# Optimization experiments

Hardware: AMD Instinct MI355X
Metric: run time of the kernel (lower is better)

## Reference

```python
import math
import jax, jax.numpy as jnp
import numpy as np

BLOCK_K = 128  # key/value block size; S_k % BLOCK_K == 0 so no padding/mask needed


def setup_inputs() -> dict:
    key = jax.random.key(0)
    kq, kk, kv = jax.random.split(key, 3)
    B, S, H, Hkv, D = 1, 4096, 16, 8, 128
    return {
        "query": jax.random.normal(kq, (B, S, H, D), dtype=jnp.float32),
        "key": jax.random.normal(kk, (B, S, Hkv, D), dtype=jnp.float32),
        "value": jax.random.normal(kv, (B, S, Hkv, D), dtype=jnp.float32),
    }


def _ring_attention(query, key, value, block_k=BLOCK_K):
    # query: [B, Sq, H, D]; key/value: [B, Sk, Hkv, D]
    scale = 1.0 / math.sqrt(query.shape[-1])
    reps = query.shape[2] // key.shape[2]
    if reps > 1:  # GQA: repeat kv heads to match query heads
        key = jnp.repeat(key, reps, axis=2)
        value = jnp.repeat(value, reps, axis=2)
    q = jnp.transpose(query, (0, 2, 1, 3))   # [B, H, Sq, D]
    k = jnp.transpose(key, (0, 2, 1, 3))     # [B, H, Sk, D]
    v = jnp.transpose(value, (0, 2, 1, 3))
    B, H, Sq, D = q.shape
    Sk = k.shape[2]
    nk = Sk // block_k
    # split keys/values into blocks, block axis leading for scan
    kb = k.reshape(B, H, nk, block_k, D).transpose(2, 0, 1, 3, 4)
    vb = v.reshape(B, H, nk, block_k, D).transpose(2, 0, 1, 3, 4)
    m0 = jnp.full((B, H, Sq), -jnp.inf, dtype=jnp.float32)
    l0 = jnp.zeros((B, H, Sq), dtype=jnp.float32)
    o0 = jnp.zeros((B, H, Sq, D), dtype=jnp.float32)

    def step(carry, kv_blk):
        m, l, o = carry
        k_blk, v_blk = kv_blk
        scores = jnp.einsum('bhqd,bhkd->bhqk', q, k_blk) * scale
        m_new = jnp.maximum(m, jnp.max(scores, axis=-1))
        alpha = jnp.exp(m - m_new)                     # rescale factor (0 on first step)
        p = jnp.exp(scores - m_new[..., None])
        l = l * alpha + jnp.sum(p, axis=-1)
        o = o * alpha[..., None] + jnp.einsum('bhqk,bhkd->bhqd', p, v_blk)
        return (m_new, l, o), None

    (m, l, o), _ = jax.lax.scan(step, (m0, l0, o0), (kb, vb))
    out = o / l[..., None]
    return jnp.transpose(out, (0, 2, 1, 3))  # [B, Sq, H, D]


def reference(query, key, value):
    return _ring_attention(query, key, value)
```

## Files before the change

kernel.cpp:

```cpp
#include <hip/hip_runtime.h>
#include <math.h>


namespace {
constexpr int NH  = 16;
constexpr int NKV = 8;
constexpr int DH  = 128;
constexpr int SK  = 4096;
constexpr int TQ  = 128;
constexpr int NT  = 256;

constexpr int BKM   = 32;
constexpr int NKTM  = SK / BKM;
constexpr int TILEM = BKM * DH;
constexpr size_t WS_NEED = (size_t)2 * NKV * NKTM * TILEM * sizeof(_Float16);

constexpr int BK  = 64;
constexpr int NKT = SK / BK;

typedef _Float16 half8 __attribute__((ext_vector_type(8)));
typedef _Float16 half4 __attribute__((ext_vector_type(4)));
typedef _Float16 half2v __attribute__((ext_vector_type(2)));
typedef __fp16   fp16x2 __attribute__((ext_vector_type(2)));
typedef float  floatx4 __attribute__((ext_vector_type(4)));
typedef unsigned short ushort8 __attribute__((ext_vector_type(8)));

#define MFMA16(a, b, c) __builtin_amdgcn_mfma_f32_16x16x32_f16((a), (b), (c), 0, 0, 0)

__global__ __launch_bounds__(256)
void prepack_kv(const float* __restrict__ Kg, const float* __restrict__ Vg,
                _Float16* __restrict__ Kx, _Float16* __restrict__ Vx) {
  __shared__ __align__(16) _Float16 Kb[BKM * 128];
  __shared__ __align__(16) _Float16 Vb[BKM * 132];
  const int id = blockIdx.x;
  const int hk = id & 7;
  const int kt = id >> 3;
  const int t  = threadIdx.x;

#pragma unroll
  for (int it = 0; it < 4; ++it) {
    const int r  = it * 8 + (t >> 5);
    const int c4 = t & 31;
    const size_t src = (((size_t)(kt * BKM + r) * NKV + hk) * DH) + c4 * 4;
    const float4 kf = *reinterpret_cast<const float4*>(Kg + src);
    const float4 vf = *reinterpret_cast<const float4*>(Vg + src);
    half4 kh;
    kh[0] = (_Float16)kf.x; kh[1] = (_Float16)kf.y;
    kh[2] = (_Float16)kf.z; kh[3] = (_Float16)kf.w;
    *reinterpret_cast<half4*>(&Kb[r * 128 + c4 * 4]) = kh;
    half2v v0, v1;
    v0[0] = (_Float16)vf.x; v0[1] = (_Float16)vf.y;
    v1[0] = (_Float16)vf.z; v1[1] = (_Float16)vf.w;
    *reinterpret_cast<half2v*>(&Vb[r * 132 + c4 * 4])     = v0;
    *reinterpret_cast<half2v*>(&Vb[r * 132 + c4 * 4 + 2]) = v1;
  }
  __syncthreads();

  {
    _Float16* out = Kx + (size_t)(hk * NKTM + kt) * TILEM;
#pragma unroll
    for (int it = 0; it < 2; ++it) {
      const int L  = it * 2048 + t * 8;
      const int r  = L >> 7;
      const int gp = (L >> 3) & 15;
      const int c8 = gp ^ (r & 7);
      *reinterpret_cast<half8*>(out + L) =
          *reinterpret_cast<const half8*>(&Kb[r * 128 + c8 * 8]);
    }
  }
  {
    _Float16* out = Vx + (size_t)(hk * NKTM + kt) * TILEM;
    const int dp = t >> 2;
    const int g  = t & 3;
    const int ql = g ^ (dp & 3);
    const int d  = dp * 2;
    ushort8 lo, hi;
#pragma unroll
    for (int j = 0; j < 8; ++j) {
      const int key = ((j >> 2) * 16) + ql * 4 + (j & 3);
      const unsigned v = *reinterpret_cast<const unsigned*>(&Vb[key * 132 + d]);
      lo[j] = (unsigned short)(v & 0xffffu);
      hi[j] = (unsigned short)(v >> 16);
    }
    *reinterpret_cast<ushort8*>(out + d * 32 + g * 8)       = lo;
    *reinterpret_cast<ushort8*>(out + (d + 1) * 32 + g * 8) = hi;
  }
}

__global__ __launch_bounds__(NT, 2)
void flash_fwd_pk(const float* __restrict__ Qg,
                  const _Float16* __restrict__ Kx,
                  const _Float16* __restrict__ Vx,
                  float* __restrict__ Og) {
  __shared__ __align__(16) _Float16 KsB[2][TILEM];
  __shared__ __align__(16) _Float16 VtB[2][TILEM];

  const int tid  = threadIdx.x;
  const int wave = tid >> 6;
  const int lane = tid & 63;
  const int m16  = lane & 15;
  const int quad = lane >> 4;
  const int hsw  = m16 & 7;
  const int sw2  = (m16 >> 1) & 3;

  const int id = blockIdx.x;
  const int hk = id & 7;
  const int h  = (hk << 1) | ((id >> 3) & 1);
  const int qt = id >> 4;
  const int qr0 = qt * TQ + wave * 32;

  const float4* Q4 = reinterpret_cast<const float4*>(Qg);
  const float scale2 = (float)(0.08838834764831845 * 1.4426950408889634);

  half8 qa[2][4];
#pragma unroll
  for (int mt = 0; mt < 2; ++mt) {
#pragma unroll
    for (int kc = 0; kc < 4; ++kc) {
      const int r = qr0 + mt * 16 + m16;
      const int b = (r * NH + h) * (DH / 4) + kc * 8 + quad * 2;
      float4 x = Q4[b], y = Q4[b + 1];
      half8 f;
      f[0] = (_Float16)(x.x * scale2); f[1] = (_Float16)(x.y * scale2);
      f[2] = (_Float16)(x.z * scale2); f[3] = (_Float16)(x.w * scale2);
      f[4] = (_Float16)(y.x * scale2); f[5] = (_Float16)(y.y * scale2);
      f[6] = (_Float16)(y.z * scale2); f[7] = (_Float16)(y.w * scale2);
      qa[mt][kc] = f;
    }
  }

  floatx4 o[2][8];
#pragma unroll
  for (int mt = 0; mt < 2; ++mt)
#pragma unroll
    for (int nt = 0; nt < 8; ++nt) o[mt][nt] = (floatx4){0.f, 0.f, 0.f, 0.f};
  float lsum[2] = {0.f, 0.f};

  const _Float16* gK = Kx + (size_t)hk * NKTM * TILEM;
  const _Float16* gV = Vx + (size_t)hk * NKTM * TILEM;
  const int soff = tid * 8;

  half8 kr[2], vr[2];
#pragma unroll
  for (int i = 0; i < 2; ++i) {
    kr[i] = *reinterpret_cast<const half8*>(gK + i * 2048 + soff);
    vr[i] = *reinterpret_cast<const half8*>(gV + i * 2048 + soff);
  }

  for (int kt = 0; kt < NKTM; ++kt) {
    const int b = kt & 1;
#pragma unroll
    for (int i = 0; i < 2; ++i) {
      *reinterpret_cast<half8*>(&KsB[b][i * 2048 + soff]) = kr[i];
      *reinterpret_cast<half8*>(&VtB[b][i * 2048 + soff]) = vr[i];
    }
    {
      const int ktn = (kt + 1 < NKTM) ? kt + 1 : kt;
      const _Float16* gKt = gK + (size_t)ktn * TILEM;
      const _Float16* gVt = gV + (size_t)ktn * TILEM;
#pragma unroll
      for (int i = 0; i < 2; ++i) {
        kr[i] = *reinterpret_cast<const half8*>(gKt + i * 2048 + soff);
        vr[i] = *reinterpret_cast<const half8*>(gVt + i * 2048 + soff);
      }
    }
    __syncthreads();

    const _Float16* Ks = KsB[b];
    const _Float16* Vt = VtB[b];

    floatx4 s[2][2];
#pragma unroll
    for (int mt = 0; mt < 2; ++mt)
#pragma unroll
      for (int nt = 0; nt < 2; ++nt) s[mt][nt] = (floatx4){0.f, 0.f, 0.f, 0.f};
#pragma unroll
    for (int nt = 0; nt < 2; ++nt) {
#pragma unroll
      for (int kc = 0; kc < 4; ++kc) {
        const int g = (kc * 4 + quad) ^ hsw;
        half8 kb = *reinterpret_cast<const half8*>(
            &Ks[(nt * 16 + m16) * 128 + g * 8]);
        s[0][nt] = MFMA16(kb, qa[0][nt * 0 + kc], s[0][nt]);
        s[1][nt] = MFMA16(kb, qa[1][kc], s[1][nt]);
      }
    }

    union H8 { half8 h; fp16x2 w[4]; };
    half8 pa[2];
#pragma unroll
    for (int mt = 0; mt < 2; ++mt) {
      float p[8];
#pragma unroll
      for (int nt = 0; nt < 2; ++nt)
#pragma unroll
        for (int r = 0; r < 4; ++r)
          p[nt * 4 + r] = __builtin_amdgcn_exp2f(s[mt][nt][r]);
      lsum[mt] += ((p[0] + p[1]) + (p[2] + p[3])) +
                  ((p[4] + p[5]) + (p[6] + p[7]));
      H8 u;
      u.w[0] = __builtin_amdgcn_cvt_pkrtz(p[0], p[1]);
      u.w[1] = __builtin_amdgcn_cvt_pkrtz(p[2], p[3]);
      u.w[2] = __builtin_amdgcn_cvt_pkrtz(p[4], p[5]);
      u.w[3] = __builtin_amdgcn_cvt_pkrtz(p[6], p[7]);
      pa[mt] = u.h;
    }

    const int gq = quad ^ sw2;
#pragma unroll
    for (int nt = 0; nt < 8; ++nt) {
      half8 vb = *reinterpret_cast<const half8*>(
          &Vt[(nt * 16 + m16) * 32 + gq * 8]);
      o[0][nt] = MFMA16(pa[0], vb, o[0][nt]);
      o[1][nt] = MFMA16(pa[1], vb, o[1][nt]);
    }
  }

#pragma unroll
  for (int mt = 0; mt < 2; ++mt) {
    float ls = lsum[mt];
    ls += __shfl_xor(ls, 16);
    ls += __shfl_xor(ls, 32);
#pragma unroll
    for (int r = 0; r < 4; ++r) {
      const int rq = quad * 4 + r;
      const float inv = 1.f / __shfl(ls, rq);
      const int row = qr0 + mt * 16 + rq;
      const int ob = (row * NH + h) * DH + m16;
#pragma unroll
      for (int nt = 0; nt < 8; ++nt)
        Og[ob + nt * 16] = o[mt][nt][r] * inv;
    }
  }
}

constexpr int KP = 136, VP = 72, PP = 72;

__global__ __launch_bounds__(NT, 2)
void flash_fwd_fb(const float* __restrict__ Qg, const float* __restrict__ Kg,
                  const float* __restrict__ Vg, float* __restrict__ Og) {
  __shared__ _Float16 Ks[BK * KP];
  __shared__ _Float16 Vt[DH * VP];
  __shared__ _Float16 Ps[4 * 32 * PP];

  const int tid  = threadIdx.x;
  const int wave = tid >> 6;
  const int lane = tid & 63;
  const int m16  = lane & 15;
  const int quad = lane >> 4;

  const int id = blockIdx.x;
  const int hk = id & 7;
  const int h  = (hk << 1) | ((id >> 3) & 1);
  const int qt = id >> 4;
  const int qr0 = qt * TQ + wave * 32;

  const float4* Q4 = reinterpret_cast<const float4*>(Qg);
  const float4* K4 = reinterpret_cast<const float4*>(Kg);
  const float scale2 = (float)(0.08838834764831845 * 1.4426950408889634);

  half8 qa[2][4];
#pragma unroll
  for (int mt = 0; mt < 2; ++mt) {
#pragma unroll
    for (int kc = 0; kc < 4; ++kc) {
      const int r = qr0 + mt * 16 + m16;
      const int b = (r * NH + h) * (DH / 4) + kc * 8 + quad * 2;
      float4 x = Q4[b], y = Q4[b + 1];
      half8 f;
      f[0] = (_Float16)(x.x * scale2); f[1] = (_Float16)(x.y * scale2);
      f[2] = (_Float16)(x.z * scale2); f[3] = (_Float16)(x.w * scale2);
      f[4] = (_Float16)(y.x * scale2); f[5] = (_Float16)(y.y * scale2);
      f[6] = (_Float16)(y.z * scale2); f[7] = (_Float16)(y.w * scale2);
      qa[mt][kc] = f;
    }
  }

  floatx4 o[2][8];
#pragma unroll
  for (int mt = 0; mt < 2; ++mt)
#pragma unroll
    for (int nt = 0; nt < 8; ++nt) o[mt][nt] = (floatx4){0.f, 0.f, 0.f, 0.f};
  float lrow[2][4];
#pragma unroll
  for (int mt = 0; mt < 2; ++mt)
#pragma unroll
    for (int r = 0; r < 4; ++r) lrow[mt][r] = 0.f;

  const int kkey = tid >> 2, kdq = tid & 3;
  const int vdim = tid & 127, vkg = tid >> 7;

  float4 kpre[8];
  float  vpre[32];
  {
    const int kb = (kkey * NKV + hk) * (DH / 4);
#pragma unroll
    for (int j = 0; j < 8; ++j) kpre[j] = K4[kb + j * 4 + kdq];
    const int vb = (vkg * 32) * NKV * DH + hk * DH + vdim;
#pragma unroll
    for (int e = 0; e < 32; ++e) vpre[e] = Vg[vb + e * (NKV * DH)];
  }

  for (int kt = 0; kt < NKT; ++kt) {
    __syncthreads();
#pragma unroll
    for (int j = 0; j < 8; ++j) {
      fp16x2 a = __builtin_amdgcn_cvt_pkrtz(kpre[j].x, kpre[j].y);
      fp16x2 b = __builtin_amdgcn_cvt_pkrtz(kpre[j].z, kpre[j].w);
      half4 hv;
      hv[0] = (_Float16)a[0]; hv[1] = (_Float16)a[1];
      hv[2] = (_Float16)b[0]; hv[3] = (_Float16)b[1];
      *reinterpret_cast<half4*>(&Ks[kkey * KP + (j * 4 + kdq) * 4]) = hv;
    }
#pragma unroll
    for (int jj = 0; jj < 4; ++jj) {
      half8 hv;
#pragma unroll
      for (int e = 0; e < 4; ++e) {
        fp16x2 p = __builtin_amdgcn_cvt_pkrtz(vpre[jj * 8 + 2 * e],
                                              vpre[jj * 8 + 2 * e + 1]);
        hv[2 * e] = (_Float16)p[0]; hv[2 * e + 1] = (_Float16)p[1];
      }
      *reinterpret_cast<half8*>(&Vt[vdim * VP + vkg * 32 + jj * 8]) = hv;
    }
    __syncthreads();

    floatx4 s[2][4];
#pragma unroll
    for (int mt = 0; mt < 2; ++mt)
#pragma unroll
      for (int nt = 0; nt < 4; ++nt) s[mt][nt] = (floatx4){0.f, 0.f, 0.f, 0.f};
#pragma unroll
    for (int nt = 0; nt < 4; ++nt) {
#pragma unroll
      for (int kc = 0; kc < 4; ++kc) {
        half8 kb = *reinterpret_cast<const half8*>(
            &Ks[(nt * 16 + m16) * KP + kc * 32 + quad * 8]);
        s[0][nt] = MFMA16(qa[0][kc], kb, s[0][nt]);
        s[1][nt] = MFMA16(qa[1][kc], kb, s[1][nt]);
      }
    }

    {
      const int ktn = (kt + 1 < NKT) ? kt + 1 : kt;
      const int kb = ((ktn * BK + kkey) * NKV + hk) * (DH / 4);
#pragma unroll
      for (int j = 0; j < 8; ++j) kpre[j] = K4[kb + j * 4 + kdq];
      const int vb = (ktn * BK + vkg * 32) * NKV * DH + hk * DH + vdim;
#pragma unroll
      for (int e = 0; e < 32; ++e) vpre[e] = Vg[vb + e * (NKV * DH)];
    }

#pragma unroll
    for (int mt = 0; mt < 2; ++mt) {
#pragma unroll
      for (int nt = 0; nt < 4; ++nt) {
#pragma unroll
        for (int r = 0; r < 4; ++r) {
          const float p = exp2f(s[mt][nt][r]);
          s[mt][nt][r] = p;
          lrow[mt][r] += p;
        }
      }
#pragma unroll
      for (int r = 0; r < 4; ++r) {
        const int prow = (wave * 32 + mt * 16 + quad * 4 + r) * PP;
#pragma unroll
        for (int nt = 0; nt < 4; ++nt)
          Ps[prow + nt * 16 + m16] = (_Float16)s[mt][nt][r];
      }
    }

    half8 pa[2][2];
#pragma unroll
    for (int mt = 0; mt < 2; ++mt)
#pragma unroll
      for (int kc = 0; kc < 2; ++kc)
        pa[mt][kc] = *reinterpret_cast<const half8*>(
            &Ps[(wave * 32 + mt * 16 + m16) * PP + kc * 32 + quad * 8]);
#pragma unroll
    for (int nt = 0; nt < 8; ++nt) {
#pragma unroll
      for (int kc = 0; kc < 2; ++kc) {
        half8 vb = *reinterpret_cast<const half8*>(
            &Vt[(nt * 16 + m16) * VP + kc * 32 + quad * 8]);
        o[0][nt] = MFMA16(pa[0][kc], vb, o[0][nt]);
        o[1][nt] = MFMA16(pa[1][kc], vb, o[1][nt]);
      }
    }
  }

#pragma unroll
  for (int mt = 0; mt < 2; ++mt) {
#pragma unroll
    for (int r = 0; r < 4; ++r) {
      float ls = lrow[mt][r];
      ls += __shfl_xor(ls, 1);
      ls += __shfl_xor(ls, 2);
      ls += __shfl_xor(ls, 4);
      ls += __shfl_xor(ls, 8);
      const float inv = 1.f / ls;
      const int row = qr0 + mt * 16 + quad * 4 + r;
      const int ob = (row * NH + h) * DH + m16;
#pragma unroll
      for (int nt = 0; nt < 8; ++nt)
        Og[ob + nt * 16] = o[mt][nt][r] * inv;
    }
  }
}
}

extern "C" void kernel_launch(void* const* d_in, const int* in_sizes, int n_in,
                              void* d_out, int out_size, void* d_ws, size_t ws_size,
                              hipStream_t stream) {
  const float* Q = (const float*)d_in[0];
  const float* K = (const float*)d_in[1];
  const float* V = (const float*)d_in[2];
  float* O = (float*)d_out;
  if (ws_size >= WS_NEED) {
    _Float16* Kx = (_Float16*)d_ws;
    _Float16* Vx = Kx + (size_t)NKV * NKTM * TILEM;
    prepack_kv<<<1024, 256, 0, stream>>>(K, V, Kx, Vx);
    flash_fwd_pk<<<512, NT, 0, stream>>>(Q, Kx, Vx, O);
  } else {
    flash_fwd_fb<<<512, NT, 0, stream>>>(Q, K, V, O);
  }
}
```

Measured before the change: 228.4 us.

## Process two K/V tiles per barrier with setprio around MFMA sections

The K/V staging loop now loads two 32-key tiles per iteration into double-buffered shared memory, which halves the number of barriers and global-load rounds. The plain __syncthreads is replaced by an inline-asm waitcnt plus s_barrier, and s_setprio raises wave priority around the MFMA blocks to encourage interleaving between waves. This doubles the LDS footprint and the prefetch registers, which may cut occupancy under launch_bounds(256,2).

```diff
diff --git a/kernel.cpp b/kernel.cpp
--- a/kernel.cpp
+++ b/kernel.cpp
@@ -15,6 +15,9 @@
 constexpr int TILEM = BKM * DH;
 constexpr size_t WS_NEED = (size_t)2 * NKV * NKTM * TILEM * sizeof(_Float16);
 
+constexpr int NIT   = NKTM / 2;
+constexpr int CHUNK = 2 * TILEM;
+
 constexpr int BK  = 64;
 constexpr int NKT = SK / BK;
 
@@ -26,6 +29,8 @@
 typedef unsigned short ushort8 __attribute__((ext_vector_type(8)));
 
 #define MFMA16(a, b, c) __builtin_amdgcn_mfma_f32_16x16x32_f16((a), (b), (c), 0, 0, 0)
+
+#define BARRIER_LGKM() asm volatile("s_waitcnt lgkmcnt(0)\n\ts_barrier" ::: "memory")
 
 __global__ __launch_bounds__(256)
 void prepack_kv(const float* __restrict__ Kg, const float* __restrict__ Vg,
@@ -92,8 +97,8 @@
                   const _Float16* __restrict__ Kx,
                   const _Float16* __restrict__ Vx,
                   float* __restrict__ Og) {
-  __shared__ __align__(16) _Float16 KsB[2][TILEM];
-  __shared__ __align__(16) _Float16 VtB[2][TILEM];
+  __shared__ __align__(16) _Float16 KsB[2][CHUNK];
+  __shared__ __align__(16) _Float16 VtB[2][CHUNK];
 
   const int tid  = threadIdx.x;
   const int wave = tid >> 6;
@@ -140,79 +145,86 @@
   const _Float16* gV = Vx + (size_t)hk * NKTM * TILEM;
   const int soff = tid * 8;
 
-  half8 kr[2], vr[2];
-#pragma unroll
-  for (int i = 0; i < 2; ++i) {
+  half8 kr[4], vr[4];
+#pragma unroll
+  for (int i = 0; i < 4; ++i) {
     kr[i] = *reinterpret_cast<const half8*>(gK + i * 2048 + soff);
     vr[i] = *reinterpret_cast<const half8*>(gV + i * 2048 + soff);
   }
 
-  for (int kt = 0; kt < NKTM; ++kt) {
+  for (int kt = 0; kt < NIT; ++kt) {
     const int b = kt & 1;
 #pragma unroll
-    for (int i = 0; i < 2; ++i) {
+    for (int i = 0; i < 4; ++i) {
       *reinterpret_cast<half8*>(&KsB[b][i * 2048 + soff]) = kr[i];
       *reinterpret_cast<half8*>(&VtB[b][i * 2048 + soff]) = vr[i];
     }
     {
-      const int ktn = (kt + 1 < NKTM) ? kt + 1 : kt;
-      const _Float16* gKt = gK + (size_t)ktn * TILEM;
-      const _Float16* gVt = gV + (size_t)ktn * TILEM;
-#pragma unroll
-      for (int i = 0; i < 2; ++i) {
+      const int ktn = (kt + 1 < NIT) ? kt + 1 : kt;
+      const _Float16* gKt = gK + (size_t)ktn * CHUNK;
+      const _Float16* gVt = gV + (size_t)ktn * CHUNK;
+#pragma unroll
+      for (int i = 0; i < 4; ++i) {
         kr[i] = *reinterpret_cast<const half8*>(gKt + i * 2048 + soff);
         vr[i] = *reinterpret_cast<const half8*>(gVt + i * 2048 + soff);
       }
     }
-    __syncthreads();
-
-    const _Float16* Ks = KsB[b];
-    const _Float16* Vt = VtB[b];
-
-    floatx4 s[2][2];
-#pragma unroll
-    for (int mt = 0; mt < 2; ++mt)
-#pragma unroll
-      for (int nt = 0; nt < 2; ++nt) s[mt][nt] = (floatx4){0.f, 0.f, 0.f, 0.f};
-#pragma unroll
-    for (int nt = 0; nt < 2; ++nt) {
-#pragma unroll
-      for (int kc = 0; kc < 4; ++kc) {
-        const int g = (kc * 4 + quad) ^ hsw;
-        half8 kb = *reinterpret_cast<const half8*>(
-            &Ks[(nt * 16 + m16) * 128 + g * 8]);
-        s[0][nt] = MFMA16(kb, qa[0][nt * 0 + kc], s[0][nt]);
-        s[1][nt] = MFMA16(kb, qa[1][kc], s[1][nt]);
-      }
-    }
-
-    union H8 { half8 h; fp16x2 w[4]; };
-    half8 pa[2];
-#pragma unroll
-    for (int mt = 0; mt < 2; ++mt) {
-      float p[8];
-#pragma unroll
-      for (int nt = 0; nt < 2; ++nt)
-#pragma unroll
-        for (int r = 0; r < 4; ++r)
-          p[nt * 4 + r] = __builtin_amdgcn_exp2f(s[mt][nt][r]);
-      lsum[mt] += ((p[0] + p[1]) + (p[2] + p[3])) +
-                  ((p[4] + p[5]) + (p[6] + p[7]));
-      H8 u;
-      u.w[0] = __builtin_amdgcn_cvt_pkrtz(p[0], p[1]);
-      u.w[1] = __builtin_amdgcn_cvt_pkrtz(p[2], p[3]);
-      u.w[2] = __builtin_amdgcn_cvt_pkrtz(p[4], p[5]);
-      u.w[3] = __builtin_amdgcn_cvt_pkrtz(p[6], p[7]);
-      pa[mt] = u.h;
-    }
-
-    const int gq = quad ^ sw2;
-#pragma unroll
-    for (int nt = 0; nt < 8; ++nt) {
-      half8 vb = *reinterpret_cast<const half8*>(
-          &Vt[(nt * 16 + m16) * 32 + gq * 8]);
-      o[0][nt] = MFMA16(pa[0], vb, o[0][nt]);
-      o[1][nt] = MFMA16(pa[1], vb, o[1][nt]);
+    BARRIER_LGKM();
+
+#pragma unroll
+    for (int c = 0; c < 2; ++c) {
+      const _Float16* Ks = &KsB[b][c * TILEM];
+      const _Float16* Vt = &VtB[b][c * TILEM];
+
+      floatx4 s[2][2];
+#pragma unroll
+      for (int mt = 0; mt < 2; ++mt)
+#pragma unroll
+        for (int nt = 0; nt < 2; ++nt) s[mt][nt] = (floatx4){0.f, 0.f, 0.f, 0.f};
+      __builtin_amdgcn_s_setprio(1);
+#pragma unroll
+      for (int nt = 0; nt < 2; ++nt) {
+#pragma unroll
+        for (int kc = 0; kc < 4; ++kc) {
+          const int g = (kc * 4 + quad) ^ hsw;
+          half8 kb = *reinterpret_cast<const half8*>(
+              &Ks[(nt * 16 + m16) * 128 + g * 8]);
+          s[0][nt] = MFMA16(kb, qa[0][kc], s[0][nt]);
+          s[1][nt] = MFMA16(kb, qa[1][kc], s[1][nt]);
+        }
+      }
+      __builtin_amdgcn_s_setprio(0);
+
+      union H8 { half8 h; fp16x2 w[4]; };
+      half8 pa[2];
+#pragma unroll
+      for (int mt = 0; mt < 2; ++mt) {
+        float p[8];
+#pragma unroll
+        for (int nt = 0; nt < 2; ++nt)
+#pragma unroll
+          for (int r = 0; r < 4; ++r)
+            p[nt * 4 + r] = __builtin_amdgcn_exp2f(s[mt][nt][r]);
+        lsum[mt] += ((p[0] + p[1]) + (p[2] + p[3])) +
+                    ((p[4] + p[5]) + (p[6] + p[7]));
+        H8 u;
+        u.w[0] = __builtin_amdgcn_cvt_pkrtz(p[0], p[1]);
+        u.w[1] = __builtin_amdgcn_cvt_pkrtz(p[2], p[3]);
+        u.w[2] = __builtin_amdgcn_cvt_pkrtz(p[4], p[5]);
+        u.w[3] = __builtin_amdgcn_cvt_pkrtz(p[6], p[7]);
+        pa[mt] = u.h;
+      }
+
+      const int gq = quad ^ sw2;
+      __builtin_amdgcn_s_setprio(1);
+#pragma unroll
+      for (int nt = 0; nt < 8; ++nt) {
+        half8 vb = *reinterpret_cast<const half8*>(
+            &Vt[(nt * 16 + m16) * 32 + gq * 8]);
+        o[0][nt] = MFMA16(pa[0], vb, o[0][nt]);
+        o[1][nt] = MFMA16(pa[1], vb, o[1][nt]);
+      }
+      __builtin_amdgcn_s_setprio(0);
     }
   }
 
```

After: 228.7 us. No clear change (+0.1%).
